# Performance work log

Hardware: AMD Instinct MI355X
Metric: run time of the kernel (lower is better)

Reference implementation:

```python
import jax, jax.numpy as jnp
import numpy as np

N_NODES = 50000
D = 128
DROP_P = 0.2


def sage_conv(x, edge_index, W_l, W_r, b):
    # PyG SAGEConv (mean aggr): out = lin_l(mean_j x_j) + lin_r(x)
    src, dst = edge_index[0], edge_index[1]
    n = x.shape[0]
    agg = jax.ops.segment_sum(x[src], dst, num_segments=n)          # [N, F]
    cnt = jax.ops.segment_sum(jnp.ones((src.shape[0],), x.dtype), dst, num_segments=n)
    mean = agg / jnp.maximum(cnt, 1.0)[:, None]
    return mean @ W_l.T + x @ W_r.T + b


def setup_inputs() -> dict:
    key = jax.random.key(0)
    ks = jax.random.split(key, 9)
    x = jax.random.normal(ks[0], (N_NODES, D), dtype=jnp.float32)
    edge_index = jax.random.randint(ks[1], (2, 800000), 0, N_NODES, dtype=jnp.int64)
    s = 1.0 / np.sqrt(D)
    W1_l = jax.random.uniform(ks[2], (D, D), jnp.float32, -s, s)
    W1_r = jax.random.uniform(ks[3], (D, D), jnp.float32, -s, s)
    b1 = jax.random.uniform(ks[4], (D,), jnp.float32, -s, s)
    W2_l = jax.random.uniform(ks[5], (D, D), jnp.float32, -s, s)
    W2_r = jax.random.uniform(ks[6], (D, D), jnp.float32, -s, s)
    b2 = jax.random.uniform(ks[7], (D,), jnp.float32, -s, s)
    return {"x": x, "edge_index": edge_index, "W1_l": W1_l, "W1_r": W1_r,
            "b1": b1, "W2_l": W2_l, "W2_r": W2_r, "b2": b2}


def reference(x, edge_index, W1_l, W1_r, b1, W2_l, W2_r, b2):
    h = sage_conv(x, edge_index, W1_l, W1_r, b1)
    h = jax.nn.relu(h)
    # F.dropout(p=0.2) defaults to training=True; deterministic fixed-key mask
    keep = jax.random.bernoulli(jax.random.key(42), 1.0 - DROP_P, h.shape)
    h = jnp.where(keep, h / (1.0 - DROP_P), 0.0)
    return sage_conv(h, edge_index, W2_l, W2_r, b2)
```

## Files before the change

### kernel.cpp

```cpp
#include <hip/hip_runtime.h>
#include <stdint.h>

#define N_NODES 50000
#define D 128
#define N_EDGES 800000
#define NBUCK 196
#define BCAP 8192
#define EPB 4096

typedef __attribute__((ext_vector_type(8))) short bf16x8;
typedef __attribute__((ext_vector_type(4))) float f32x4;

__device__ __forceinline__ unsigned short f2bf(float f){
  unsigned u = __float_as_uint(f);
  u = u + 0x7FFFu + ((u >> 16) & 1u);
  return (unsigned short)(u >> 16);
}
__device__ __forceinline__ void acc2(float& a, float& b, unsigned w){
  a += __uint_as_float(w << 16);
  b += __uint_as_float(w & 0xFFFF0000u);
}

__device__ __forceinline__ unsigned rotl32(unsigned x, int r){
  return (x << r) | (x >> (32 - r));
}
__device__ __forceinline__ float dropout_factor(unsigned idx){
  unsigned x0 = 0u, x1 = idx;
  const unsigned ks0 = 0u;
  const unsigned ks1 = 42u;
  const unsigned ks2 = 0x1BD11BDAu ^ 0u ^ 42u;
  x0 += ks0; x1 += ks1;
  #define TFR(r) { x0 += x1; x1 = rotl32(x1,(r)); x1 ^= x0; }
  TFR(13) TFR(15) TFR(26) TFR(6)   x0 += ks1; x1 += ks2 + 1u;
  TFR(17) TFR(29) TFR(16) TFR(24)  x0 += ks2; x1 += ks0 + 2u;
  TFR(13) TFR(15) TFR(26) TFR(6)   x0 += ks0; x1 += ks1 + 3u;
  TFR(17) TFR(29) TFR(16) TFR(24)  x0 += ks1; x1 += ks2 + 4u;
  TFR(13) TFR(15) TFR(26) TFR(6)   x0 += ks2; x1 += ks0 + 5u;
  #undef TFR
  unsigned bits = x0 ^ x1;
  float u = __uint_as_float(0x3F800000u | (bits >> 9)) - 1.0f;
  return (u < 0.8f) ? 1.25f : 0.0f;
}

__global__ __launch_bounds__(256) void prep_bucket_kernel(
    const float* __restrict__ x,
    const float* __restrict__ W1l, const float* __restrict__ W1r,
    const float* __restrict__ W2l, const float* __restrict__ W2r,
    unsigned short* __restrict__ A1cat,
    unsigned short* __restrict__ Wcat1, unsigned short* __restrict__ Wcat2,
    const void* __restrict__ ei, int* __restrict__ gcursor, int* __restrict__ buck)
{
  int b = blockIdx.x, t = threadIdx.x;
  if (b < 6250){
    int i = b * 256 + t;
    int r = i >> 5, c4 = (i & 31) * 4;
    float4 v = *(const float4*)(x + (size_t)r * 128 + c4);
    ushort4 o = make_ushort4(f2bf(v.x), f2bf(v.y), f2bf(v.z), f2bf(v.w));
    *(ushort4*)(A1cat + (size_t)r * 256 + 128 + c4) = o;
    return;
  }
  if (b < 6506){
    int c = (b < 6378) ? (b - 6250) : (b - 6378);
    const float* Wl = (b < 6378) ? W1l : W2l;
    const float* Wr = (b < 6378) ? W1r : W2r;
    unsigned short* Wc = (b < 6378) ? Wcat1 : Wcat2;
    float v = (t < 128) ? Wl[c * 128 + t] : Wr[c * 128 + (t - 128)];
    Wc[c * 256 + t] = f2bf(v);
    return;
  }
  __shared__ int hist[NBUCK];
  __shared__ int baseoff[NBUCK];
  __shared__ int nz;
  const int bb = b - 6506;
  const int base = bb * EPB;
  if (t == 0) nz = 0;
  for (int i = t; i < NBUCK; i += 256) hist[i] = 0;
  __syncthreads();
  {
    const int* p = (const int*)ei;
    int local = 0;
    for (int i = t; i < 1024; i += 256)
      if (p[2 * i + 1] != 0) local = 1;
    if (local) atomicAdd(&nz, 1);
  }
  __syncthreads();
  const int is64 = (nz == 0);

  int pk[16], bk[16], rk[16];
  #pragma unroll
  for (int j = 0; j < 16; ++j) bk[j] = -1;

  if (is64){
    const long long* p = (const long long*)ei;
    #pragma unroll
    for (int k = 0; k < 8; ++k){
      int e = base + (k * 256 + t) * 2;
      if (e < N_EDGES){
        int4 vs = *(const int4*)(p + e);
        int4 vd = *(const int4*)(p + N_EDGES + e);
        int j0 = k * 2, j1 = k * 2 + 1;
        bk[j0] = vd.x >> 8; pk[j0] = (vs.x << 8) | (vd.x & 255);
        rk[j0] = atomicAdd(&hist[bk[j0]], 1);
        bk[j1] = vd.z >> 8; pk[j1] = (vs.z << 8) | (vd.z & 255);
        rk[j1] = atomicAdd(&hist[bk[j1]], 1);
      }
    }
  } else {
    const int* p = (const int*)ei;
    #pragma unroll
    for (int k = 0; k < 4; ++k){
      int e = base + (k * 256 + t) * 4;
      if (e < N_EDGES){
        int4 vs = *(const int4*)(p + e);
        int4 vd = *(const int4*)(p + N_EDGES + e);
        int ss[4] = {vs.x, vs.y, vs.z, vs.w};
        int dd[4] = {vd.x, vd.y, vd.z, vd.w};
        #pragma unroll
        for (int j = 0; j < 4; ++j){
          int slot = k * 4 + j;
          bk[slot] = dd[j] >> 8;
          pk[slot] = (ss[j] << 8) | (dd[j] & 255);
          rk[slot] = atomicAdd(&hist[bk[slot]], 1);
        }
      }
    }
  }
  __syncthreads();
  for (int i = t; i < NBUCK; i += 256){
    int h = hist[i];
    baseoff[i] = h ? atomicAdd(&gcursor[i], h) : 0;
  }
  __syncthreads();
  #pragma unroll
  for (int j = 0; j < 16; ++j){
    if (bk[j] >= 0)
      buck[bk[j] * BCAP + baseoff[bk[j]] + rk[j]] = pk[j];
  }
}

__global__ __launch_bounds__(256) void csr_kernel(const int* __restrict__ gcursor,
                                                  const int* __restrict__ buck,
                                                  unsigned short* __restrict__ csr16,
                                                  int* __restrict__ rowptr){
  __shared__ int sb[256];
  __shared__ int h[256];
  __shared__ int s[256];
  __shared__ int cur[256];
  const int b = blockIdx.x, t = threadIdx.x;
  sb[t] = (t < NBUCK) ? gcursor[t] : 0;
  __syncthreads();
  #pragma unroll
  for (int off = 1; off < 256; off <<= 1){
    int u = (t >= off) ? sb[t - off] : 0;
    __syncthreads();
    sb[t] += u;
    __syncthreads();
  }
  const int gbase = (b == 0) ? 0 : sb[b - 1];
  const int cntb  = gcursor[b];
  h[t] = 0;
  __syncthreads();
  for (int i = t; i < cntb; i += 256)
    atomicAdd(&h[buck[b * BCAP + i] & 255], 1);
  __syncthreads();
  s[t] = h[t];
  __syncthreads();
  #pragma unroll
  for (int off = 1; off < 256; off <<= 1){
    int u = (t >= off) ? s[t - off] : 0;
    __syncthreads();
    s[t] += u;
    __syncthreads();
  }
  int excl = s[t] - h[t];
  int node = b * 256 + t;
  if (node < N_NODES) rowptr[node] = gbase + excl;
  if (b == 0 && t == 0) rowptr[N_NODES] = N_EDGES;
  cur[t] = gbase + excl;
  __syncthreads();
  for (int i = t; i < cntb; i += 256){
    int pkv = buck[b * BCAP + i];
    int pos = atomicAdd(&cur[pkv & 255], 1);
    csr16[pos] = (unsigned short)(((unsigned)pkv) >> 8);
  }
}

__global__ __launch_bounds__(256) void agg_bf16_kernel(
    unsigned short* __restrict__ Acat, const int* __restrict__ rowptr,
    const unsigned short* __restrict__ csr16)
{
  int node = blockIdx.x * 4 + (threadIdx.x >> 6);
  int lane = threadIdx.x & 63;
  if (node >= N_NODES) return;
  int q  = lane >> 4;
  int fl = lane & 15;
  int e0 = rowptr[node], e1 = rowptr[node + 1];
  float s0=0.f,s1=0.f,s2=0.f,s3=0.f,s4=0.f,s5=0.f,s6=0.f,s7=0.f;

  int e = e0;
  for (; e + 16 <= e1; e += 16){
    int i0 = csr16[e + q];
    int i1 = csr16[e + 4 + q];
    int i2 = csr16[e + 8 + q];
    int i3 = csr16[e + 12 + q];
    int4 v0 = *(const int4*)(Acat + (size_t)i0 * 256 + 128 + fl * 8);
    int4 v1 = *(const int4*)(Acat + (size_t)i1 * 256 + 128 + fl * 8);
    int4 v2 = *(const int4*)(Acat + (size_t)i2 * 256 + 128 + fl * 8);
    int4 v3 = *(const int4*)(Acat + (size_t)i3 * 256 + 128 + fl * 8);
    acc2(s0, s1, (unsigned)v0.x); acc2(s2, s3, (unsigned)v0.y);
    acc2(s4, s5, (unsigned)v0.z); acc2(s6, s7, (unsigned)v0.w);
    acc2(s0, s1, (unsigned)v1.x); acc2(s2, s3, (unsigned)v1.y);
    acc2(s4, s5, (unsigned)v1.z); acc2(s6, s7, (unsigned)v1.w);
    acc2(s0, s1, (unsigned)v2.x); acc2(s2, s3, (unsigned)v2.y);
    acc2(s4, s5, (unsigned)v2.z); acc2(s6, s7, (unsigned)v2.w);
    acc2(s0, s1, (unsigned)v3.x); acc2(s2, s3, (unsigned)v3.y);
    acc2(s4, s5, (unsigned)v3.z); acc2(s6, s7, (unsigned)v3.w);
  }
  for (; e + 8 <= e1; e += 8){
    int i0 = csr16[e + q];
    int i1 = csr16[e + 4 + q];
    int4 v0 = *(const int4*)(Acat + (size_t)i0 * 256 + 128 + fl * 8);
    int4 v1 = *(const int4*)(Acat + (size_t)i1 * 256 + 128 + fl * 8);
    acc2(s0, s1, (unsigned)v0.x); acc2(s2, s3, (unsigned)v0.y);
    acc2(s4, s5, (unsigned)v0.z); acc2(s6, s7, (unsigned)v0.w);
    acc2(s0, s1, (unsigned)v1.x); acc2(s2, s3, (unsigned)v1.y);
    acc2(s4, s5, (unsigned)v1.z); acc2(s6, s7, (unsigned)v1.w);
  }
  for (; e < e1; e += 4){
    int ee = e + q;
    if (ee < e1){
      int i0 = csr16[ee];
      int4 v0 = *(const int4*)(Acat + (size_t)i0 * 256 + 128 + fl * 8);
      acc2(s0, s1, (unsigned)v0.x); acc2(s2, s3, (unsigned)v0.y);
      acc2(s4, s5, (unsigned)v0.z); acc2(s6, s7, (unsigned)v0.w);
    }
  }
  s0 += __shfl_xor(s0, 16); s0 += __shfl_xor(s0, 32);
  s1 += __shfl_xor(s1, 16); s1 += __shfl_xor(s1, 32);
  s2 += __shfl_xor(s2, 16); s2 += __shfl_xor(s2, 32);
  s3 += __shfl_xor(s3, 16); s3 += __shfl_xor(s3, 32);
  s4 += __shfl_xor(s4, 16); s4 += __shfl_xor(s4, 32);
  s5 += __shfl_xor(s5, 16); s5 += __shfl_xor(s5, 32);
  s6 += __shfl_xor(s6, 16); s6 += __shfl_xor(s6, 32);
  s7 += __shfl_xor(s7, 16); s7 += __shfl_xor(s7, 32);
  if (q == 0){
    float inv = 1.0f / fmaxf((float)(e1 - e0), 1.0f);
    unsigned short ob[8] = { f2bf(s0*inv), f2bf(s1*inv), f2bf(s2*inv), f2bf(s3*inv),
                             f2bf(s4*inv), f2bf(s5*inv), f2bf(s6*inv), f2bf(s7*inv) };
    int4 o;
    o.x = (unsigned)ob[0] | ((unsigned)ob[1] << 16);
    o.y = (unsigned)ob[2] | ((unsigned)ob[3] << 16);
    o.z = (unsigned)ob[4] | ((unsigned)ob[5] << 16);
    o.w = (unsigned)ob[6] | ((unsigned)ob[7] << 16);
    *(int4*)(Acat + (size_t)node * 256 + fl * 8) = o;
  }
}

__global__ __launch_bounds__(256) void gemm_mfma(
    const unsigned short* __restrict__ Acat, const unsigned short* __restrict__ Wcat,
    const float* __restrict__ bias, void* __restrict__ outp, int mode)
{
  __shared__ __align__(16) char smem[64 * 132 * 4];
  const int t   = threadIdx.x;
  const int w   = t >> 6;
  const int tl  = t & 63;
  const int m15 = tl & 15;
  const int q   = tl >> 4;
  const int row0 = blockIdx.x * 64;

  bf16x8 bfr[2][8];
  #pragma unroll
  for (int ct = 0; ct < 2; ++ct){
    int col = w * 32 + ct * 16 + m15;
    #pragma unroll
    for (int kc = 0; kc < 8; ++kc)
      bfr[ct][kc] = *(const bf16x8*)(Wcat + (size_t)col * 256 + kc * 32 + q * 8);
  }

  #pragma unroll
  for (int u = 0; u < 8; ++u){
    int g   = t + 256 * u;
    int row = g >> 5, ch = g & 31;
    int kc  = ch >> 2, qq = ch & 3;
    int f   = (row >> 4) * 8 + kc;
    int slot = (row & 15) + 16 * qq;
    int gr = row0 + row; if (gr > N_NODES - 1) gr = N_NODES - 1;
    int4 v = *(const int4*)((const char*)Acat + (size_t)gr * 512 + ch * 16);
    *(int4*)(smem + (size_t)(f * 64 + (slot ^ kc)) * 16) = v;
  }
  __syncthreads();

  f32x4 acc[4][2];
  #pragma unroll
  for (int rt = 0; rt < 4; ++rt)
    #pragma unroll
    for (int ct = 0; ct < 2; ++ct)
      acc[rt][ct] = (f32x4){0.f, 0.f, 0.f, 0.f};

  #pragma unroll
  for (int kc = 0; kc < 8; ++kc){
    bf16x8 a[4];
    #pragma unroll
    for (int rt = 0; rt < 4; ++rt)
      a[rt] = *(const bf16x8*)(smem + (size_t)((rt * 8 + kc) * 64 + (tl ^ kc)) * 16);
    #pragma unroll
    for (int rt = 0; rt < 4; ++rt)
      #pragma unroll
      for (int ct = 0; ct < 2; ++ct)
        acc[rt][ct] = __builtin_amdgcn_mfma_f32_16x16x32_bf16(a[rt], bfr[ct][kc], acc[rt][ct], 0, 0, 0);
  }
  __syncthreads();

  float* sf = (float*)smem;
  #pragma unroll
  for (int rt = 0; rt < 4; ++rt)
    #pragma unroll
    for (int ct = 0; ct < 2; ++ct)
      #pragma unroll
      for (int i = 0; i < 4; ++i){
        int row = rt * 16 + q * 4 + i;
        int col = w * 32 + ct * 16 + m15;
        sf[row * 132 + col] = acc[rt][ct][i];
      }
  __syncthreads();

  if (mode == 1){
    unsigned short* hout = (unsigned short*)outp;
    #pragma unroll
    for (int v = 0; v < 4; ++v){
      int s = t + 256 * v;
      int row = s >> 4, c8 = (s & 15) * 8;
      int gr = row0 + row;
      if (gr < N_NODES){
        float4 p0 = *(const float4*)&sf[row * 132 + c8];
        float4 p1 = *(const float4*)&sf[row * 132 + c8 + 4];
        float vals[8] = {p0.x, p0.y, p0.z, p0.w, p1.x, p1.y, p1.z, p1.w};
        unsigned short ob[8];
        #pragma unroll
        for (int j = 0; j < 8; ++j){
          float vv = vals[j] + bias[c8 + j];
          vv = fmaxf(vv, 0.0f);
          vv *= dropout_factor((unsigned)(gr * 128 + c8 + j));
          ob[j] = f2bf(vv);
        }
        int4 o;
        o.x = (unsigned)ob[0] | ((unsigned)ob[1] << 16);
        o.y = (unsigned)ob[2] | ((unsigned)ob[3] << 16);
        o.z = (unsigned)ob[4] | ((unsigned)ob[5] << 16);
        o.w = (unsigned)ob[6] | ((unsigned)ob[7] << 16);
        *(int4*)(hout + (size_t)gr * 256 + 128 + c8) = o;
      }
    }
  } else {
    float* of = (float*)outp;
    #pragma unroll
    for (int v = 0; v < 8; ++v){
      int s = t + 256 * v;
      int row = s >> 5, c4 = (s & 31) * 4;
      int gr = row0 + row;
      if (gr < N_NODES){
        float4 p = *(const float4*)&sf[row * 132 + c4];
        p.x += bias[c4 + 0]; p.y += bias[c4 + 1];
        p.z += bias[c4 + 2]; p.w += bias[c4 + 3];
        *(float4*)(of + (size_t)gr * 128 + c4) = p;
      }
    }
  }
}

extern "C" void kernel_launch(void* const* d_in, const int* in_sizes, int n_in,
                              void* d_out, int out_size, void* d_ws, size_t ws_size,
                              hipStream_t stream)
{
  const float* x   = (const float*)d_in[0];
  const void*  ei  = d_in[1];
  const float* W1l = (const float*)d_in[2];
  const float* W1r = (const float*)d_in[3];
  const float* b1  = (const float*)d_in[4];
  const float* W2l = (const float*)d_in[5];
  const float* W2r = (const float*)d_in[6];
  const float* b2  = (const float*)d_in[7];

  char* ws = (char*)d_ws;
  unsigned short* A1cat = (unsigned short*)ws;
  size_t off = (size_t)N_NODES * 256 * sizeof(unsigned short);
  int* rowptr      = (int*)(ws + off);  off += (size_t)(N_NODES + 1) * sizeof(int);
  off = (off + 15) & ~(size_t)15;
  unsigned short* csr16 = (unsigned short*)(ws + off); off += (size_t)N_EDGES * sizeof(unsigned short);
  int* gcursor     = (int*)(ws + off);  off += NBUCK * sizeof(int);
  off = (off + 15) & ~(size_t)15;
  int* buck        = (int*)(ws + off);  off += (size_t)NBUCK * BCAP * sizeof(int);
  unsigned short* Wcat1 = (unsigned short*)(ws + off); off += 128 * 256 * sizeof(unsigned short);
  unsigned short* Wcat2 = (unsigned short*)(ws + off); off += 128 * 256 * sizeof(unsigned short);

  unsigned short* A2cat = (unsigned short*)d_out;

  hipMemsetAsync(gcursor, 0, NBUCK * sizeof(int), stream);
  prep_bucket_kernel<<<6702, 256, 0, stream>>>(x, W1l, W1r, W2l, W2r, A1cat,
                                               Wcat1, Wcat2, ei, gcursor, buck);
  csr_kernel<<<NBUCK, 256, 0, stream>>>(gcursor, buck, csr16, rowptr);

  agg_bf16_kernel<<<(N_NODES + 3) / 4, 256, 0, stream>>>(A1cat, rowptr, csr16);
  gemm_mfma<<<(N_NODES + 63) / 64, 256, 0, stream>>>(A1cat, Wcat1, b1, (void*)A2cat, 1);
  agg_bf16_kernel<<<(N_NODES + 3) / 4, 256, 0, stream>>>(A2cat, rowptr, csr16);
  gemm_mfma<<<(N_NODES + 63) / 64, 256, 0, stream>>>(A2cat, Wcat2, b2, d_out, 0);

  (void)in_sizes; (void)n_in; (void)out_size; (void)ws_size;
}
```

Measured before the change: 218.6 us.

## Precompute dropout bitmask in prep kernel instead of layer-1 GEMM epilogue

Threefry-based dropout mask generation moves out of the layer-1 GEMM epilogue into extra blocks of the prep/bucketing kernel, interleaved one in nine. Each thread packs 32 keep bits into a word stored in a 782x256 word workspace mask. The GEMM epilogue then reads one mask word per 8 outputs and applies the 1.25 scale. This takes the RNG ALU work off the GEMM critical path and lets it overlap with the memory-bound prep work, at the cost of extra blocks, a small mask write/read, and a div/mod in block dispatch.

```diff
diff --git a/kernel.cpp b/kernel.cpp
--- a/kernel.cpp
+++ b/kernel.cpp
@@ -7,6 +7,7 @@
 #define NBUCK 196
 #define BCAP 8192
 #define EPB 4096
+#define NDROP 782
 
 typedef __attribute__((ext_vector_type(8))) short bf16x8;
 typedef __attribute__((ext_vector_type(4))) float f32x4;
@@ -24,7 +25,7 @@
 __device__ __forceinline__ unsigned rotl32(unsigned x, int r){
   return (x << r) | (x >> (32 - r));
 }
-__device__ __forceinline__ float dropout_factor(unsigned idx){
+__device__ __forceinline__ int dropout_keep(unsigned idx){
   unsigned x0 = 0u, x1 = idx;
   const unsigned ks0 = 0u;
   const unsigned ks1 = 42u;
@@ -39,7 +40,7 @@
   #undef TFR
   unsigned bits = x0 ^ x1;
   float u = __uint_as_float(0x3F800000u | (bits >> 9)) - 1.0f;
-  return (u < 0.8f) ? 1.25f : 0.0f;
+  return (u < 0.8f) ? 1 : 0;
 }
 
 __global__ __launch_bounds__(256) void prep_bucket_kernel(
@@ -48,22 +49,35 @@
     const float* __restrict__ W2l, const float* __restrict__ W2r,
     unsigned short* __restrict__ A1cat,
     unsigned short* __restrict__ Wcat1, unsigned short* __restrict__ Wcat2,
-    const void* __restrict__ ei, int* __restrict__ gcursor, int* __restrict__ buck)
+    const void* __restrict__ ei, int* __restrict__ gcursor, int* __restrict__ buck,
+    unsigned* __restrict__ dmask)
 {
   int b = blockIdx.x, t = threadIdx.x;
-  if (b < 6250){
-    int i = b * 256 + t;
-    int r = i >> 5, c4 = (i & 31) * 4;
-    float4 v = *(const float4*)(x + (size_t)r * 128 + c4);
+  int g = b / 9, r = b % 9;
+  if (r == 8 && g < NDROP){
+    unsigned base = (unsigned)(g * 8192 + t * 32);
+    unsigned w = 0;
+    #pragma unroll 2
+    for (int j = 0; j < 32; ++j)
+      w |= ((unsigned)dropout_keep(base + j)) << j;
+    dmask[g * 256 + t] = w;
+    return;
+  }
+  int L = b - ((g < NDROP) ? g : NDROP);
+
+  if (L < 6250){
+    int i = L * 256 + t;
+    int rr = i >> 5, c4 = (i & 31) * 4;
+    float4 v = *(const float4*)(x + (size_t)rr * 128 + c4);
     ushort4 o = make_ushort4(f2bf(v.x), f2bf(v.y), f2bf(v.z), f2bf(v.w));
-    *(ushort4*)(A1cat + (size_t)r * 256 + 128 + c4) = o;
+    *(ushort4*)(A1cat + (size_t)rr * 256 + 128 + c4) = o;
     return;
   }
-  if (b < 6506){
-    int c = (b < 6378) ? (b - 6250) : (b - 6378);
-    const float* Wl = (b < 6378) ? W1l : W2l;
-    const float* Wr = (b < 6378) ? W1r : W2r;
-    unsigned short* Wc = (b < 6378) ? Wcat1 : Wcat2;
+  if (L < 6506){
+    int c = (L < 6378) ? (L - 6250) : (L - 6378);
+    const float* Wl = (L < 6378) ? W1l : W2l;
+    const float* Wr = (L < 6378) ? W1r : W2r;
+    unsigned short* Wc = (L < 6378) ? Wcat1 : Wcat2;
     float v = (t < 128) ? Wl[c * 128 + t] : Wr[c * 128 + (t - 128)];
     Wc[c * 256 + t] = f2bf(v);
     return;
@@ -71,7 +85,7 @@
   __shared__ int hist[NBUCK];
   __shared__ int baseoff[NBUCK];
   __shared__ int nz;
-  const int bb = b - 6506;
+  const int bb = L - 6506;
   const int base = bb * EPB;
   if (t == 0) nz = 0;
   for (int i = t; i < NBUCK; i += 256) hist[i] = 0;
@@ -258,7 +272,8 @@
 
 __global__ __launch_bounds__(256) void gemm_mfma(
     const unsigned short* __restrict__ Acat, const unsigned short* __restrict__ Wcat,
-    const float* __restrict__ bias, void* __restrict__ outp, int mode)
+    const float* __restrict__ bias, const unsigned* __restrict__ dmask,
+    void* __restrict__ outp, int mode)
 {
   __shared__ __align__(16) char smem[64 * 132 * 4];
   const int t   = threadIdx.x;
@@ -335,13 +350,14 @@
         float4 p0 = *(const float4*)&sf[row * 132 + c8];
         float4 p1 = *(const float4*)&sf[row * 132 + c8 + 4];
         float vals[8] = {p0.x, p0.y, p0.z, p0.w, p1.x, p1.y, p1.z, p1.w};
+        unsigned mw = dmask[gr * 4 + (c8 >> 5)];
         unsigned short ob[8];
         #pragma unroll
         for (int j = 0; j < 8; ++j){
           float vv = vals[j] + bias[c8 + j];
           vv = fmaxf(vv, 0.0f);
-          vv *= dropout_factor((unsigned)(gr * 128 + c8 + j));
-          ob[j] = f2bf(vv);
+          float keep = ((mw >> ((c8 & 31) + j)) & 1u) ? 1.25f : 0.0f;
+          ob[j] = f2bf(vv * keep);
         }
         int4 o;
         o.x = (unsigned)ob[0] | ((unsigned)ob[1] << 16);
@@ -392,18 +408,20 @@
   int* buck        = (int*)(ws + off);  off += (size_t)NBUCK * BCAP * sizeof(int);
   unsigned short* Wcat1 = (unsigned short*)(ws + off); off += 128 * 256 * sizeof(unsigned short);
   unsigned short* Wcat2 = (unsigned short*)(ws + off); off += 128 * 256 * sizeof(unsigned short);
+  unsigned* dmask  = (unsigned*)(ws + off); off += (size_t)NDROP * 256 * sizeof(unsigned);
 
   unsigned short* A2cat = (unsigned short*)d_out;
 
   hipMemsetAsync(gcursor, 0, NBUCK * sizeof(int), stream);
-  prep_bucket_kernel<<<6702, 256, 0, stream>>>(x, W1l, W1r, W2l, W2r, A1cat,
-                                               Wcat1, Wcat2, ei, gcursor, buck);
+  prep_bucket_kernel<<<6702 + NDROP, 256, 0, stream>>>(x, W1l, W1r, W2l, W2r, A1cat,
+                                                       Wcat1, Wcat2, ei, gcursor, buck,
+                                                       dmask);
   csr_kernel<<<NBUCK, 256, 0, stream>>>(gcursor, buck, csr16, rowptr);
 
   agg_bf16_kernel<<<(N_NODES + 3) / 4, 256, 0, stream>>>(A1cat, rowptr, csr16);
-  gemm_mfma<<<(N_NODES + 63) / 64, 256, 0, stream>>>(A1cat, Wcat1, b1, (void*)A2cat, 1);
+  gemm_mfma<<<(N_NODES + 63) / 64, 256, 0, stream>>>(A1cat, Wcat1, b1, dmask, (void*)A2cat, 1);
   agg_bf16_kernel<<<(N_NODES + 3) / 4, 256, 0, stream>>>(A2cat, rowptr, csr16);
-  gemm_mfma<<<(N_NODES + 63) / 64, 256, 0, stream>>>(A2cat, Wcat2, b2, d_out, 0);
+  gemm_mfma<<<(N_NODES + 63) / 64, 256, 0, stream>>>(A2cat, Wcat2, b2, dmask, d_out, 0);
 
   (void)in_sizes; (void)n_in; (void)out_size; (void)ws_size;
 }
```

Result: faster. 212.3 us (-2.9%).
